# Performance work log

Measured on AMD Instinct MI355X. Metric: run time of the kernel, lower is better.

## Reference

```python
import jax, jax.numpy as jnp
import numpy as np

B, M, K, KNN = 2, 256, 64, 16
CXYZ, CFEAT = 3, 61
CIN = CXYZ + CFEAT  # 64
MLPS = [64, 128]
SUMM = sum(MLPS)    # 192
CALIB = 64
EXP = [256, 512]
OUT = 256
EPS = 1e-5


def bn(x, g, b):
    # BatchNorm eval mode with running_mean=0, running_var=1 (channel axis 1)
    shape = (1, -1) + (1,) * (x.ndim - 2)
    return x * (g / jnp.sqrt(1.0 + EPS)).reshape(shape) + b.reshape(shape)


def knn(x, k):
    xx = jnp.sum(x * x, axis=1)                      # (B, N)
    inner = jnp.einsum('bcn,bcm->bnm', x, x)         # (B, N, N)
    pd = 2.0 * inner - xx[:, :, None] - xx[:, None, :]
    return jax.lax.top_k(pd, k)[1]                   # (B, N, k)


def graph_feature(x, idx):
    # x: (B, C, N), idx: (B, N, k) -> (B, 2C, N, k)
    xt = jnp.transpose(x, (0, 2, 1))                 # (B, N, C)
    nb = jax.vmap(lambda a, i: a[i])(xt, idx)        # (B, N, k, C)
    ctr = xt[:, :, None, :]
    feat = jnp.concatenate([nb - ctr, jnp.broadcast_to(ctr, nb.shape)], axis=-1)
    return jnp.transpose(feat, (0, 3, 1, 2))


def forward(xyz, feats, e1_w, e1_g, e1_b, e2_w, e2_g, e2_b,
            cal1_w, cal1_g, cal1_b, cal2_w, cal2_bias,
            exp1_w, exp1_g, exp1_b, exp2_w, exp2_g, exp2_b,
            red_w, red_g, red_b, sc1_w, sc1_b, sc2_w, sc2_b,
            sc_n1_g, sc_n1_b, sc_n2_g, sc_n2_b):
    x3 = xyz.reshape(B * M, K, CXYZ).transpose(0, 2, 1)      # (BM, 3, K)
    f = feats.reshape(B * M, K, CFEAT).transpose(0, 2, 1)    # (BM, 61, K)
    idx = knn(x3, KNN)                                        # USE_FEATS_DIS=False: knn once on xyz
    x = jnp.concatenate([x3, f], axis=1)                      # (BM, 64, K)
    outs = []
    for W, g, b in ((e1_w, e1_g, e1_b), (e2_w, e2_g, e2_b)):
        gf = graph_feature(x, idx)                            # (BM, 2C, K, knn)
        y = jax.nn.relu(bn(jnp.einsum('oc,bcnk->bonk', W, gf), g, b))
        x = y.max(axis=-1)                                    # (BM, mlp_i, K)
        outs.append(x)
    x = jnp.concatenate(outs, axis=1)                         # (BM, 192, K)
    c = jax.nn.relu(bn(jnp.einsum('oc,bcn->bon', cal1_w, x), cal1_g, cal1_b))
    c = jnp.einsum('oc,bcn->bon', cal2_w, c) + cal2_bias[None, :, None]
    x = jax.nn.sigmoid(c) * x
    x = jax.nn.relu(bn(jnp.einsum('oc,bcn->bon', exp1_w, x), exp1_g, exp1_b))
    x = jax.nn.relu(bn(jnp.einsum('oc,bcn->bon', exp2_w, x), exp2_g, exp2_b))
    x = x.max(axis=-1).reshape(B, M, EXP[1]).transpose(0, 2, 1)  # (B, 512, M)
    x = jax.nn.relu(bn(jnp.einsum('oc,bcm->bom', red_w, x), red_g, red_b))
    x = bn(x + x, sc_n1_g, sc_n1_b)
    h = jax.nn.relu(jnp.einsum('oc,bcm->bom', sc1_w, x) + sc1_b[None, :, None])
    h = jnp.einsum('oc,bcm->bom', sc2_w, h) + sc2_b[None, :, None]
    x = bn(x + h, sc_n2_g, sc_n2_b)
    return x                                                  # (B, 256, M)


def setup_inputs() -> dict:
    key = jax.random.key(0)
    ks = jax.random.split(key, 16)
    w = lambda k, s: jax.random.normal(k, s, jnp.float32) * 0.05
    ones = lambda n: jnp.ones((n,), jnp.float32)
    zeros = lambda n: jnp.zeros((n,), jnp.float32)
    return {
        'xyz': jax.random.normal(ks[0], (B, M, K, CXYZ), jnp.float32),
        'feats': jax.random.normal(ks[1], (B, M, K, CFEAT), jnp.float32),
        'e1_w': w(ks[2], (MLPS[0], 2 * CIN)), 'e1_g': ones(MLPS[0]), 'e1_b': zeros(MLPS[0]),
        'e2_w': w(ks[3], (MLPS[1], 2 * MLPS[0])), 'e2_g': ones(MLPS[1]), 'e2_b': zeros(MLPS[1]),
        'cal1_w': w(ks[4], (CALIB, SUMM)), 'cal1_g': ones(CALIB), 'cal1_b': zeros(CALIB),
        'cal2_w': w(ks[5], (SUMM, CALIB)), 'cal2_bias': zeros(SUMM),
        'exp1_w': w(ks[6], (EXP[0], SUMM)), 'exp1_g': ones(EXP[0]), 'exp1_b': zeros(EXP[0]),
        'exp2_w': w(ks[7], (EXP[1], EXP[0])), 'exp2_g': ones(EXP[1]), 'exp2_b': zeros(EXP[1]),
        'red_w': w(ks[8], (OUT, EXP[1])), 'red_g': ones(OUT), 'red_b': zeros(OUT),
        'sc1_w': w(ks[9], (OUT, OUT)), 'sc1_b': zeros(OUT),
        'sc2_w': w(ks[10], (OUT, OUT)), 'sc2_b': zeros(OUT),
        'sc_n1_g': ones(OUT), 'sc_n1_b': zeros(OUT),
        'sc_n2_g': ones(OUT), 'sc_n2_b': zeros(OUT),
    }


def reference(xyz, feats, e1_w, e1_g, e1_b, e2_w, e2_g, e2_b,
              cal1_w, cal1_g, cal1_b, cal2_w, cal2_bias,
              exp1_w, exp1_g, exp1_b, exp2_w, exp2_g, exp2_b,
              red_w, red_g, red_b, sc1_w, sc1_b, sc2_w, sc2_b,
              sc_n1_g, sc_n1_b, sc_n2_g, sc_n2_b):
    return forward(xyz, feats, e1_w, e1_g, e1_b, e2_w, e2_g, e2_b,
                   cal1_w, cal1_g, cal1_b, cal2_w, cal2_bias,
                   exp1_w, exp1_g, exp1_b, exp2_w, exp2_g, exp2_b,
                   red_w, red_g, red_b, sc1_w, sc1_b, sc2_w, sc2_b,
                   sc_n1_g, sc_n1_b, sc_n2_g, sc_n2_b)
```

## Files before the change

kernel.cpp:

```cpp
#include <hip/hip_runtime.h>
#include <hip/hip_bf16.h>
#include <math.h>
#include <stddef.h>

#define DEV __device__ __forceinline__
__device__ const float BNS = 0.99999500003749968f;

typedef __bf16 bf16x8 __attribute__((ext_vector_type(8)));
typedef float  f32x4  __attribute__((ext_vector_type(4)));

#define MF(a,b,c) __builtin_amdgcn_mfma_f32_16x16x32_bf16(a,b,c,0,0,0)

DEV unsigned short f2bs(float v){
  union{ __hip_bfloat16 b; unsigned short u; } c; c.b=__float2bfloat16(v); return c.u;
}
DEV float bs2f(unsigned short u){
  union{ unsigned short u; __hip_bfloat16 b; } c; c.u=u; return __bfloat162float(c.b);
}

DEV void put_split(unsigned short* chunks, int n, int c, float v){
  unsigned short hv=f2bs(v), lv=f2bs(v-bs2f(hv));
  int cc=c>>5, u=(c>>3)&3, e=c&7;
  unsigned short* base = chunks + cc*4096;
  base[(n*8 + (u     ^ (n&7)))*8 + e] = hv;
  base[(n*8 + ((u+4) ^ (n&7)))*8 + e] = lv;
}
DEV float get_split(const unsigned short* chunks, int n, int c){
  int cc=c>>5, u=(c>>3)&3, e=c&7;
  const unsigned short* base = chunks + cc*4096;
  return bs2f(base[(n*8 + (u     ^ (n&7)))*8 + e])
       + bs2f(base[(n*8 + ((u+4) ^ (n&7)))*8 + e]);
}


__global__ __launch_bounds__(256) void k_prep(const float* __restrict__ e1_w,
    const float* __restrict__ e2_w, const float* __restrict__ cal1_w,
    const float* __restrict__ cal2_w, const float* __restrict__ exp1_w,
    const float* __restrict__ exp2_w, unsigned short* __restrict__ Whi,
    unsigned short* __restrict__ Wlo,
    const float* __restrict__ red_w, const float* __restrict__ sc1_w,
    const float* __restrict__ sc2_w, float* __restrict__ Wt_red,
    float* __restrict__ Wt_s1, float* __restrict__ Wt_s2){
  __shared__ float s[32][33];
  int bid = blockIdx.x;
  if(bid < 896){
    const float* src; unsigned short *hi,*lo; int mode, O=0, i0;
    if(bid<32)      { src=e1_w;  hi=Whi;       lo=Wlo;       mode=1; O= 64; i0=bid*256; }
    else if(bid<96) { src=e2_w;  hi=Whi+8192;  lo=Wlo+8192;  mode=1; O=128; i0=(bid-32)*256; }
    else if(bid<144){ src=cal1_w;hi=Whi+24576; lo=Wlo+24576; mode=0;        i0=(bid-96)*256; }
    else if(bid<192){ src=cal2_w;hi=Whi+36864; lo=Wlo+36864; mode=0;        i0=(bid-144)*256; }
    else if(bid<384){ src=exp1_w;hi=Whi+49152; lo=Wlo+49152; mode=0;        i0=(bid-192)*256; }
    else            { src=exp2_w;hi=Whi+98304; lo=Wlo+98304; mode=0;        i0=(bid-384)*256; }
    int i = i0 + threadIdx.x;
    float v;
    if(mode==0) v = src[i];
    else {
      int row=i>>6, c=i&63;
      v = (row<O) ? src[row*128+c] : (src[(row-O)*128+64+c]-src[(row-O)*128+c]);
    }
    unsigned short h=f2bs(v); hi[i]=h; lo[i]=f2bs(v-bs2f(h));
  } else {
    int lb = bid-896;
    const float* in; float* out; int O,K;
    if(lb<128){ in=red_w; out=Wt_red; O=256; K=512; }
    else if(lb<192){ in=sc1_w; out=Wt_s1; O=256; K=256; lb-=128; }
    else { in=sc2_w; out=Wt_s2; O=256; K=256; lb-=192; }
    int nt=O>>5;
    int to=lb%nt, tk=lb/nt;
    int c=threadIdx.x&31, r8=threadIdx.x>>5;
    #pragma unroll
    for(int p=0;p<4;p++){
      int r=r8+p*8;
      s[r][c]=in[(size_t)(to*32+r)*K + tk*32 + c];
    }
    __syncthreads();
    #pragma unroll
    for(int p=0;p<4;p++){
      int r=r8+p*8;
      out[(size_t)(tk*32+r)*O + to*32 + c]=s[c][r];
    }
  }
}

__global__ __launch_bounds__(256) void k_knne12(const float* __restrict__ xyz,
    const float* __restrict__ feats,
    const unsigned short* __restrict__ W1h, const unsigned short* __restrict__ W1l,
    const unsigned short* __restrict__ W2h, const unsigned short* __restrict__ W2l,
    const float* __restrict__ g1, const float* __restrict__ b1,
    const float* __restrict__ g2, const float* __restrict__ b2,
    unsigned short* __restrict__ cat){
  __shared__ float bufA[64*65];
  __shared__ float bufB[64*65];
  __shared__ __align__(16) unsigned short sb[64*136];
  __shared__ int   ips[64*16];
  __shared__ float sx0[64], sx1[64], sx2[64], sxx[64];
  int bm = blockIdx.x;
  int tid = threadIdx.x, n = tid&63, s = tid>>6;
  int wid = tid>>6, lane = tid&63;
  int l15 = lane&15, q = lane>>4;
  if(s==0){
    const float* xp = xyz + (size_t)(bm*64+n)*3;
    float px=xp[0], py=xp[1], pz=xp[2];
    sx0[n]=px; sx1[n]=py; sx2[n]=pz; sxx[n]=px*px+py*py+pz*pz;
  }
  __syncthreads();
  {
    int p = lane>>2, seg = lane&3;
    int n1 = wid*16 + p;
    float px=sx0[n1], py=sx1[n1], pz=sx2[n1], xxn=sxx[n1];
    float pdr[16];
    #pragma unroll
    for(int t=0;t<16;t++){
      int m = seg*16+t;
      pdr[t] = 2.f*(px*sx0[m]+py*sx1[m]+pz*sx2[m]) - xxn - sxx[m];
    }
    for(int j=0;j<16;j++){
      float bv=-3.4e38f; int bi=seg*16;
      #pragma unroll
      for(int t=0;t<16;t++){ if(pdr[t]>bv){bv=pdr[t]; bi=seg*16+t;} }
      float ov=__shfl_xor(bv,1); int oi=__shfl_xor(bi,1);
      if(ov>bv || (ov==bv && oi<bi)){bv=ov;bi=oi;}
      ov=__shfl_xor(bv,2); oi=__shfl_xor(bi,2);
      if(ov>bv || (ov==bv && oi<bi)){bv=ov;bi=oi;}
      if(seg==0) ips[n1*16+j]=bi;
      if((bi>>4)==seg) pdr[bi&15]=-3.4e38f;
    }
  }
  {
    unsigned short* r = sb + n*136;
    if(s==0){
      float px=sx0[n], py=sx1[n], pz=sx2[n];
      unsigned short h;
      h=f2bs(px); r[0]=h; r[64]=f2bs(px-bs2f(h));
      h=f2bs(py); r[1]=h; r[65]=f2bs(py-bs2f(h));
      h=f2bs(pz); r[2]=h; r[66]=f2bs(pz-bs2f(h));
    }
    const float* fp = feats + (size_t)(bm*64+n)*61;
    #pragma unroll
    for(int t=0;t<16;t++){
      int cc = s*16+t;
      if(cc<61){
        float v=fp[cc]; unsigned short h=f2bs(v);
        r[3+cc]=h; r[64+3+cc]=f2bs(v-bs2f(h));
      }
    }
  }
  __syncthreads();
  {
    int rbase = ((wid<2)?0:64) + (wid&1)*32;
    f32x4 acc[2][4];
    #pragma unroll
    for(int a=0;a<2;a++)
      #pragma unroll
      for(int d=0;d<4;d++) acc[a][d]=(f32x4){0.f,0.f,0.f,0.f};
    #pragma unroll
    for(int kc=0;kc<2;kc++){
      int k0=kc*32;
      size_t a0=(size_t)(rbase+l15)*64 + k0 + q*8;
      size_t a1=(size_t)(rbase+16+l15)*64 + k0 + q*8;
      bf16x8 a0h=*(const bf16x8*)(W1h+a0), a0l=*(const bf16x8*)(W1l+a0);
      bf16x8 a1h=*(const bf16x8*)(W1h+a1), a1l=*(const bf16x8*)(W1l+a1);
      #pragma unroll
      for(int nt=0;nt<4;nt++){
        int row = nt*16 + l15;
        bf16x8 bh = *(const bf16x8*)&sb[row*136 + k0 + q*8];
        bf16x8 bl = *(const bf16x8*)&sb[row*136 + 64 + k0 + q*8];
        acc[0][nt]=MF(a0h,bh,acc[0][nt]);
        acc[0][nt]=MF(a0h,bl,acc[0][nt]);
        acc[0][nt]=MF(a0l,bh,acc[0][nt]);
        acc[1][nt]=MF(a1h,bh,acc[1][nt]);
        acc[1][nt]=MF(a1h,bl,acc[1][nt]);
        acc[1][nt]=MF(a1l,bh,acc[1][nt]);
      }
    }
    __syncthreads();
    float* dst = (wid<2)? bufA : bufB;
    int ro = (wid&1)*32;
    #pragma unroll
    for(int mt=0;mt<2;mt++)
      #pragma unroll
      for(int nt=0;nt<4;nt++)
        #pragma unroll
        for(int rr=0;rr<4;rr++)
          dst[(ro+mt*16+q*4+rr)*65 + nt*16+l15] = acc[mt][nt][rr];
  }
  __syncthreads();
  {
    int o = lane;
    float sc = g1[o]*BNS, bi = b1[o];
    #pragma unroll 4
    for(int j=0;j<16;j++){
      int nn = wid*16 + j;
      const int* ip = &ips[nn*16];
      float mz = -3.4e38f;
      #pragma unroll
      for(int k=0;k<16;k++) mz = fmaxf(mz, bufA[o*65 + ip[k]]);
      float v = fmaxf(sc*(mz + bufB[o*65 + nn]) + bi, 0.f);
      unsigned short hv = f2bs(v), lv = f2bs(v - bs2f(hv));
      size_t cb = ((size_t)bm*64+nn)*384 + o;
      cat[cb] = hv; cat[cb+192] = lv;
      sb[nn*136 + o] = hv; sb[nn*136 + 64 + o] = lv;
    }
  }
  for(int ch=0; ch<2; ch++){
    __syncthreads();
    int rbase = ((wid<2)?0:128) + ch*64 + (wid&1)*32;
    f32x4 acc[2][4];
    #pragma unroll
    for(int a=0;a<2;a++)
      #pragma unroll
      for(int d=0;d<4;d++) acc[a][d]=(f32x4){0.f,0.f,0.f,0.f};
    #pragma unroll
    for(int kc=0;kc<2;kc++){
      int k0=kc*32;
      size_t a0=(size_t)(rbase+l15)*64 + k0 + q*8;
      size_t a1=(size_t)(rbase+16+l15)*64 + k0 + q*8;
      bf16x8 a0h=*(const bf16x8*)(W2h+a0), a0l=*(const bf16x8*)(W2l+a0);
      bf16x8 a1h=*(const bf16x8*)(W2h+a1), a1l=*(const bf16x8*)(W2l+a1);
      #pragma unroll
      for(int nt=0;nt<4;nt++){
        int row = nt*16 + l15;
        bf16x8 bh = *(const bf16x8*)&sb[row*136 + k0 + q*8];
        bf16x8 bl = *(const bf16x8*)&sb[row*136 + 64 + k0 + q*8];
        acc[0][nt]=MF(a0h,bh,acc[0][nt]);
        acc[0][nt]=MF(a0h,bl,acc[0][nt]);
        acc[0][nt]=MF(a0l,bh,acc[0][nt]);
        acc[1][nt]=MF(a1h,bh,acc[1][nt]);
        acc[1][nt]=MF(a1h,bl,acc[1][nt]);
        acc[1][nt]=MF(a1l,bh,acc[1][nt]);
      }
    }
    __syncthreads();
    float* dst = (wid<2)? bufA : bufB;
    int ro = (wid&1)*32;
    #pragma unroll
    for(int mt=0;mt<2;mt++)
      #pragma unroll
      for(int nt=0;nt<4;nt++)
        #pragma unroll
        for(int rr=0;rr<4;rr++)
          dst[(ro+mt*16+q*4+rr)*65 + nt*16+l15] = acc[mt][nt][rr];
    __syncthreads();
    int o = ch*64 + lane;
    float sc = g2[o]*BNS, bi = b2[o];
    #pragma unroll 4
    for(int j=0;j<16;j++){
      int nn = wid*16 + j;
      const int* ip = &ips[nn*16];
      float mz = -3.4e38f;
      #pragma unroll
      for(int k=0;k<16;k++) mz = fmaxf(mz, bufA[lane*65 + ip[k]]);
      float v = fmaxf(sc*(mz + bufB[lane*65 + nn]) + bi, 0.f);
      unsigned short hv = f2bs(v);
      size_t cb = ((size_t)bm*64+nn)*384 + 64 + o;
      cat[cb] = hv; cat[cb+192] = f2bs(v - bs2f(hv));
    }
  }
}

__global__ __launch_bounds__(512,4) void k_mlp(
    const unsigned short* __restrict__ Whi, const unsigned short* __restrict__ Wlo,
    const unsigned short* __restrict__ cats,
    const float* __restrict__ c1g, const float* __restrict__ c1b,
    const float* __restrict__ c2bias,
    const float* __restrict__ e1g, const float* __restrict__ e1b,
    const float* __restrict__ e2g, const float* __restrict__ e2b,
    float* __restrict__ pool){
  __shared__ __align__(16) unsigned short buf[8*4096];
  __shared__ __align__(16) unsigned short calB[2*4096];
  int bm = blockIdx.x;
  int tid = threadIdx.x, wid = tid>>6, lane = tid&63;
  int l15 = lane&15, q = lane>>4;
  size_t xb = (size_t)bm*24576;
  #pragma unroll
  for(int i=0;i<6;i++){
    int U = tid + i*512;
    int kc = U>>9, w = U&511, rr = w>>3, up = w&7, u = up ^ (rr&7);
    const unsigned short* src = cats + xb + (size_t)rr*384
      + (u<4 ? (kc*32 + u*8) : (192 + kc*32 + (u-4)*8));
    *(uint4*)&buf[kc*4096 + w*8] = *(const uint4*)src;
  }
  __syncthreads();
  {
    int ot = wid>>1, rh = wid&1;
    f32x4 a0={0.f,0.f,0.f,0.f}, a1={0.f,0.f,0.f,0.f};
    const unsigned short* wh = Whi + 24576;
    const unsigned short* wl = Wlo + 24576;
    #pragma unroll
    for(int kc=0;kc<6;kc++){
      size_t wo = (size_t)(ot*16+l15)*192 + kc*32 + q*8;
      bf16x8 ah=*(const bf16x8*)(wh+wo), al=*(const bf16x8*)(wl+wo);
      const unsigned short* cb = buf + kc*4096;
      int r0 = rh*32+l15, r1 = rh*32+16+l15;
      bf16x8 xh0=*(const bf16x8*)&cb[(r0*8+((  q)^(r0&7)))*8];
      bf16x8 xl0=*(const bf16x8*)&cb[(r0*8+((4+q)^(r0&7)))*8];
      bf16x8 xh1=*(const bf16x8*)&cb[(r1*8+((  q)^(r1&7)))*8];
      bf16x8 xl1=*(const bf16x8*)&cb[(r1*8+((4+q)^(r1&7)))*8];
      a0=MF(ah,xh0,a0); a1=MF(ah,xh1,a1);
      a0=MF(ah,xl0,a0); a1=MF(ah,xl1,a1);
      a0=MF(al,xh0,a0); a1=MF(al,xh1,a1);
    }
    float s[4], bb[4];
    #pragma unroll
    for(int rr=0;rr<4;rr++){ int c=ot*16+q*4+rr; s[rr]=c1g[c]*BNS; bb[rr]=c1b[c]; }
    #pragma unroll
    for(int rr=0;rr<4;rr++){
      int c=ot*16+q*4+rr;
      put_split(calB, rh*32+l15,    c, fmaxf(a0[rr]*s[rr]+bb[rr],0.f));
      put_split(calB, rh*32+16+l15, c, fmaxf(a1[rr]*s[rr]+bb[rr],0.f));
    }
  }
  __syncthreads();
  {
    f32x4 ac[6];
    #pragma unroll
    for(int i=0;i<6;i++) ac[i]=(f32x4){0.f,0.f,0.f,0.f};
    const unsigned short* wh = Whi + 36864;
    const unsigned short* wl = Wlo + 36864;
    #pragma unroll
    for(int kc=0;kc<2;kc++){
      const unsigned short* cb = calB + kc*4096;
      #pragma unroll
      for(int i=0;i<6;i++){
        int j = wid*6+i, ot=j>>2, nf=j&3;
        size_t wo=(size_t)(ot*16+l15)*64 + kc*32 + q*8;
        bf16x8 ah=*(const bf16x8*)(wh+wo), al=*(const bf16x8*)(wl+wo);
        int r=nf*16+l15;
        bf16x8 xh=*(const bf16x8*)&cb[(r*8+((  q)^(r&7)))*8];
        bf16x8 xl=*(const bf16x8*)&cb[(r*8+((4+q)^(r&7)))*8];
        ac[i]=MF(ah,xh,ac[i]); ac[i]=MF(ah,xl,ac[i]); ac[i]=MF(al,xh,ac[i]);
      }
    }
    #pragma unroll
    for(int i=0;i<6;i++){
      int j=wid*6+i, ot=j>>2, nf=j&3, n=nf*16+l15;
      #pragma unroll
      for(int rr=0;rr<4;rr++){
        int c=ot*16+q*4+rr;
        float gv = 1.f/(1.f+__expf(-(ac[i][rr]+c2bias[c])));
        put_split(buf, n, c, get_split(buf,n,c)*gv);
      }
    }
  }
  __syncthreads();
  {
    f32x4 ac[2][4];
    #pragma unroll
    for(int a=0;a<2;a++)
      #pragma unroll
      for(int d=0;d<4;d++) ac[a][d]=(f32x4){0.f,0.f,0.f,0.f};
    const unsigned short* wh=Whi+49152; const unsigned short* wl=Wlo+49152;
    int ob = wid*32;
    #pragma unroll 2
    for(int kc=0;kc<6;kc++){
      bf16x8 ah[2], al[2];
      #pragma unroll
      for(int mt=0;mt<2;mt++){
        size_t wo=(size_t)(ob+mt*16+l15)*192 + kc*32 + q*8;
        ah[mt]=*(const bf16x8*)(wh+wo); al[mt]=*(const bf16x8*)(wl+wo);
      }
      const unsigned short* cb = buf + kc*4096;
      #pragma unroll
      for(int nf=0;nf<4;nf++){
        int r=nf*16+l15;
        bf16x8 xh=*(const bf16x8*)&cb[(r*8+((  q)^(r&7)))*8];
        bf16x8 xl=*(const bf16x8*)&cb[(r*8+((4+q)^(r&7)))*8];
        ac[0][nf]=MF(ah[0],xh,ac[0][nf]); ac[1][nf]=MF(ah[1],xh,ac[1][nf]);
        ac[0][nf]=MF(ah[0],xl,ac[0][nf]); ac[1][nf]=MF(ah[1],xl,ac[1][nf]);
        ac[0][nf]=MF(al[0],xh,ac[0][nf]); ac[1][nf]=MF(al[1],xh,ac[1][nf]);
      }
    }
    __syncthreads();
    #pragma unroll
    for(int mt=0;mt<2;mt++){
      float s[4], bb[4];
      #pragma unroll
      for(int rr=0;rr<4;rr++){ int c=ob+mt*16+q*4+rr; s[rr]=e1g[c]*BNS; bb[rr]=e1b[c]; }
      #pragma unroll
      for(int nf=0;nf<4;nf++){
        int n=nf*16+l15;
        #pragma unroll
        for(int rr=0;rr<4;rr++){
          int c=ob+mt*16+q*4+rr;
          put_split(buf, n, c, fmaxf(ac[mt][nf][rr]*s[rr]+bb[rr],0.f));
        }
      }
    }
  }
  __syncthreads();
  {
    f32x4 ac[4][4];
    #pragma unroll
    for(int a=0;a<4;a++)
      #pragma unroll
      for(int d=0;d<4;d++) ac[a][d]=(f32x4){0.f,0.f,0.f,0.f};
    const unsigned short* wh=Whi+98304; const unsigned short* wl=Wlo+98304;
    int ob = wid*64;
    for(int kc=0;kc<8;kc++){
      bf16x8 ah[4], al[4];
      #pragma unroll
      for(int mt=0;mt<4;mt++){
        size_t wo=(size_t)(ob+mt*16+l15)*256 + kc*32 + q*8;
        ah[mt]=*(const bf16x8*)(wh+wo); al[mt]=*(const bf16x8*)(wl+wo);
      }
      const unsigned short* cb = buf + kc*4096;
      #pragma unroll
      for(int nf=0;nf<4;nf++){
        int r=nf*16+l15;
        bf16x8 xh=*(const bf16x8*)&cb[(r*8+((  q)^(r&7)))*8];
        bf16x8 xl=*(const bf16x8*)&cb[(r*8+((4+q)^(r&7)))*8];
        #pragma unroll
        for(int mt=0;mt<4;mt++) ac[mt][nf]=MF(ah[mt],xh,ac[mt][nf]);
        #pragma unroll
        for(int mt=0;mt<4;mt++) ac[mt][nf]=MF(ah[mt],xl,ac[mt][nf]);
        #pragma unroll
        for(int mt=0;mt<4;mt++) ac[mt][nf]=MF(al[mt],xh,ac[mt][nf]);
      }
    }
    int b = bm>>8, m = bm&255;
    #pragma unroll
    for(int mt=0;mt<4;mt++){
      float s[4], bb[4];
      #pragma unroll
      for(int rr=0;rr<4;rr++){ int c=ob+mt*16+q*4+rr; s[rr]=e2g[c]*BNS; bb[rr]=e2b[c]; }
      #pragma unroll
      for(int rr=0;rr<4;rr++){
        float v = ac[mt][0][rr]*s[rr]+bb[rr];
        v = fmaxf(v, ac[mt][1][rr]*s[rr]+bb[rr]);
        v = fmaxf(v, ac[mt][2][rr]*s[rr]+bb[rr]);
        v = fmaxf(v, ac[mt][3][rr]*s[rr]+bb[rr]);
        v = fmaxf(v, 0.f);
        v = fmaxf(v, __shfl_xor(v,1));
        v = fmaxf(v, __shfl_xor(v,2));
        v = fmaxf(v, __shfl_xor(v,4));
        v = fmaxf(v, __shfl_xor(v,8));
        if(l15==0) pool[((size_t)b*512 + ob+mt*16+q*4+rr)*256 + m] = v;
      }
    }
  }
}

__global__ __launch_bounds__(512) void k_headf(const float* __restrict__ Wt_red,
    const float* __restrict__ Wt_s1, const float* __restrict__ Wt_s2,
    const float* __restrict__ pool, float* __restrict__ Og,
    const float* __restrict__ red_g, const float* __restrict__ red_b,
    const float* __restrict__ n1g, const float* __restrict__ n1b,
    const float* __restrict__ s1b, const float* __restrict__ s2b,
    const float* __restrict__ n2g, const float* __restrict__ n2b){
  __shared__ float P[512*3];
  __shared__ float X1[256*3];
  __shared__ float H[256*3];
  __shared__ float PB[256*5];
  int g = blockIdx.x;
  int b = g>>7, mg = g&127;
  int m0 = mg*2;
  int tid = threadIdx.x;
  int o = tid&255, h = tid>>8;
  {
    int c = tid;
    float2 v = *(const float2*)&pool[((size_t)b*512+c)*256 + m0];
    P[c*3+0]=v.x; P[c*3+1]=v.y;
  }
  __syncthreads();
  float a0=0.f, a1=0.f;
  {
    int c0 = h*256;
    #pragma unroll 8
    for(int i=0;i<256;i++){
      int c = c0+i;
      float w = Wt_red[c*256+o];
      a0 += w*P[c*3]; a1 += w*P[c*3+1];
    }
  }
  PB[o*5+h*2]=a0; PB[o*5+h*2+1]=a1;
  __syncthreads();
  a0 = PB[o*5]+PB[o*5+2]; a1 = PB[o*5+1]+PB[o*5+3];
  float x0r,x1r;
  {
    float s=red_g[o]*BNS, bi=red_b[o], s1=n1g[o]*BNS, b1=n1b[o];
    float r0=fmaxf(a0*s+bi,0.f), r1=fmaxf(a1*s+bi,0.f);
    x0r=2.f*r0*s1+b1; x1r=2.f*r1*s1+b1;
    if(h==0){ X1[o*3]=x0r; X1[o*3+1]=x1r; }
  }
  __syncthreads();
  a0=0.f; a1=0.f;
  {
    int c0 = h*128;
    #pragma unroll 8
    for(int i=0;i<128;i++){
      int c = c0+i;
      float w = Wt_s1[c*256+o];
      a0 += w*X1[c*3]; a1 += w*X1[c*3+1];
    }
  }
  PB[o*5+h*2]=a0; PB[o*5+h*2+1]=a1;
  __syncthreads();
  a0 = PB[o*5]+PB[o*5+2]; a1 = PB[o*5+1]+PB[o*5+3];
  {
    float bi=s1b[o];
    if(h==0){ H[o*3]=fmaxf(a0+bi,0.f); H[o*3+1]=fmaxf(a1+bi,0.f); }
  }
  __syncthreads();
  a0=0.f; a1=0.f;
  {
    int c0 = h*128;
    #pragma unroll 8
    for(int i=0;i<128;i++){
      int c = c0+i;
      float w = Wt_s2[c*256+o];
      a0 += w*H[c*3]; a1 += w*H[c*3+1];
    }
  }
  PB[o*5+h*2]=a0; PB[o*5+h*2+1]=a1;
  __syncthreads();
  if(h==0){
    a0 = PB[o*5]+PB[o*5+2]; a1 = PB[o*5+1]+PB[o*5+3];
    float bi=s2b[o], s2=n2g[o]*BNS, b2=n2b[o];
    float v0=(x0r+a0+bi)*s2+b2, v1=(x1r+a1+bi)*s2+b2;
    *(float2*)&Og[((size_t)b*256+o)*256 + m0] = make_float2(v0,v1);
  }
}

extern "C" void kernel_launch(void* const* d_in, const int* in_sizes, int n_in,
                              void* d_out, int out_size, void* d_ws, size_t ws_size,
                              hipStream_t stream){
  const float* xyz     =(const float*)d_in[0];
  const float* feats   =(const float*)d_in[1];
  const float* e1_w    =(const float*)d_in[2];
  const float* e1_g    =(const float*)d_in[3];
  const float* e1_b    =(const float*)d_in[4];
  const float* e2_w    =(const float*)d_in[5];
  const float* e2_g    =(const float*)d_in[6];
  const float* e2_b    =(const float*)d_in[7];
  const float* cal1_w  =(const float*)d_in[8];
  const float* cal1_g  =(const float*)d_in[9];
  const float* cal1_b  =(const float*)d_in[10];
  const float* cal2_w  =(const float*)d_in[11];
  const float* cal2_bias=(const float*)d_in[12];
  const float* exp1_w  =(const float*)d_in[13];
  const float* exp1_g  =(const float*)d_in[14];
  const float* exp1_b  =(const float*)d_in[15];
  const float* exp2_w  =(const float*)d_in[16];
  const float* exp2_g  =(const float*)d_in[17];
  const float* exp2_b  =(const float*)d_in[18];
  const float* red_w   =(const float*)d_in[19];
  const float* red_g   =(const float*)d_in[20];
  const float* red_b   =(const float*)d_in[21];
  const float* sc1_w   =(const float*)d_in[22];
  const float* sc1_b   =(const float*)d_in[23];
  const float* sc2_w   =(const float*)d_in[24];
  const float* sc2_b   =(const float*)d_in[25];
  const float* sc_n1_g =(const float*)d_in[26];
  const float* sc_n1_b =(const float*)d_in[27];
  const float* sc_n2_g =(const float*)d_in[28];
  const float* sc_n2_b =(const float*)d_in[29];

  char* wsb=(char*)d_ws;
  unsigned short* cats=(unsigned short*)(wsb + 10485760);
  float*          pool=(float*)         (wsb + 69206016);
  unsigned short* Whi =(unsigned short*)(wsb + 75497472);
  unsigned short* Wlo =(unsigned short*)(wsb + 76021760);
  float*          Wt_red=(float*)       (wsb + 76546048);
  float*          Wt_s1 =(float*)       (wsb + 77070336);
  float*          Wt_s2 =(float*)       (wsb + 77332480);
  unsigned short* e1e_h=Whi;          unsigned short* e1e_l=Wlo;
  unsigned short* e2e_h=Whi+8192;     unsigned short* e2e_l=Wlo+8192;

  k_prep      <<<1152,256,0,stream>>>(e1_w,e2_w,cal1_w,cal2_w,exp1_w,exp2_w,Whi,Wlo,
                                      red_w,sc1_w,sc2_w,Wt_red,Wt_s1,Wt_s2);
  k_knne12    <<<512,256,0,stream>>>(xyz,feats,e1e_h,e1e_l,e2e_h,e2e_l,
                                     e1_g,e1_b,e2_g,e2_b,cats);
  k_mlp       <<<512,512,0,stream>>>(Whi,Wlo,cats,cal1_g,cal1_b,cal2_bias,
                                     exp1_g,exp1_b,exp2_g,exp2_b,pool);
  k_headf     <<<256,512,0,stream>>>(Wt_red,Wt_s1,Wt_s2,pool,(float*)d_out,
                                     red_g,red_b,sc_n1_g,sc_n1_b,sc1_b,sc2_b,sc_n2_g,sc_n2_b);
}
```

Measured before the change: 267.5 us.

## Prefetch weight fragments across k_mlp stages and vectorize split-bf16 LDS stores

Measured after the change: 264.7 us. No clear change (-1.1%).

```diff
diff --git a/kernel.cpp b/kernel.cpp
--- a/kernel.cpp
+++ b/kernel.cpp
@@ -18,18 +18,23 @@
   union{ unsigned short u; __hip_bfloat16 b; } c; c.u=u; return __bfloat162float(c.b);
 }
 
-DEV void put_split(unsigned short* chunks, int n, int c, float v){
-  unsigned short hv=f2bs(v), lv=f2bs(v-bs2f(hv));
-  int cc=c>>5, u=(c>>3)&3, e=c&7;
+DEV void put_split4(unsigned short* chunks, int n, int c0, const float* v){
+  int cc=c0>>5, u=(c0>>3)&3, e=c0&7;
   unsigned short* base = chunks + cc*4096;
-  base[(n*8 + (u     ^ (n&7)))*8 + e] = hv;
-  base[(n*8 + ((u+4) ^ (n&7)))*8 + e] = lv;
-}
-DEV float get_split(const unsigned short* chunks, int n, int c){
-  int cc=c>>5, u=(c>>3)&3, e=c&7;
+  unsigned short h0=f2bs(v[0]), h1=f2bs(v[1]), h2=f2bs(v[2]), h3=f2bs(v[3]);
+  ushort4 hq = make_ushort4(h0,h1,h2,h3);
+  ushort4 lq = make_ushort4(f2bs(v[0]-bs2f(h0)), f2bs(v[1]-bs2f(h1)),
+                            f2bs(v[2]-bs2f(h2)), f2bs(v[3]-bs2f(h3)));
+  *(ushort4*)&base[(n*8 + (u     ^ (n&7)))*8 + e] = hq;
+  *(ushort4*)&base[(n*8 + ((u+4) ^ (n&7)))*8 + e] = lq;
+}
+DEV void get_split4(const unsigned short* chunks, int n, int c0, float* v){
+  int cc=c0>>5, u=(c0>>3)&3, e=c0&7;
   const unsigned short* base = chunks + cc*4096;
-  return bs2f(base[(n*8 + (u     ^ (n&7)))*8 + e])
-       + bs2f(base[(n*8 + ((u+4) ^ (n&7)))*8 + e]);
+  ushort4 hq = *(const ushort4*)&base[(n*8 + (u     ^ (n&7)))*8 + e];
+  ushort4 lq = *(const ushort4*)&base[(n*8 + ((u+4) ^ (n&7)))*8 + e];
+  v[0]=bs2f(hq.x)+bs2f(lq.x); v[1]=bs2f(hq.y)+bs2f(lq.y);
+  v[2]=bs2f(hq.z)+bs2f(lq.z); v[3]=bs2f(hq.w)+bs2f(lq.w);
 }
 
 
@@ -271,6 +276,14 @@
   int bm = blockIdx.x;
   int tid = threadIdx.x, wid = tid>>6, lane = tid&63;
   int l15 = lane&15, q = lane>>4;
+
+  const unsigned short* w1h = Whi + 24576;
+  const unsigned short* w1l = Wlo + 24576;
+  int c1ot = wid>>1, c1rh = wid&1;
+  size_t c1wo0 = (size_t)(c1ot*16+l15)*192 + q*8;
+  bf16x8 cah = *(const bf16x8*)(w1h+c1wo0);
+  bf16x8 cal_ = *(const bf16x8*)(w1l+c1wo0);
+
   size_t xb = (size_t)bm*24576;
   #pragma unroll
   for(int i=0;i<6;i++){
@@ -281,83 +294,115 @@
     *(uint4*)&buf[kc*4096 + w*8] = *(const uint4*)src;
   }
   __syncthreads();
-  {
-    int ot = wid>>1, rh = wid&1;
-    f32x4 a0={0.f,0.f,0.f,0.f}, a1={0.f,0.f,0.f,0.f};
-    const unsigned short* wh = Whi + 24576;
-    const unsigned short* wl = Wlo + 24576;
+
+  f32x4 a0={0.f,0.f,0.f,0.f}, a1={0.f,0.f,0.f,0.f};
+  {
+    int r0 = c1rh*32+l15, r1 = c1rh*32+16+l15;
+    __builtin_amdgcn_s_setprio(1);
     #pragma unroll
     for(int kc=0;kc<6;kc++){
-      size_t wo = (size_t)(ot*16+l15)*192 + kc*32 + q*8;
-      bf16x8 ah=*(const bf16x8*)(wh+wo), al=*(const bf16x8*)(wl+wo);
+      bf16x8 nah, nal;
+      if(kc<5){
+        size_t wo = c1wo0 + (kc+1)*32;
+        nah=*(const bf16x8*)(w1h+wo); nal=*(const bf16x8*)(w1l+wo);
+      }
       const unsigned short* cb = buf + kc*4096;
-      int r0 = rh*32+l15, r1 = rh*32+16+l15;
       bf16x8 xh0=*(const bf16x8*)&cb[(r0*8+((  q)^(r0&7)))*8];
       bf16x8 xl0=*(const bf16x8*)&cb[(r0*8+((4+q)^(r0&7)))*8];
       bf16x8 xh1=*(const bf16x8*)&cb[(r1*8+((  q)^(r1&7)))*8];
       bf16x8 xl1=*(const bf16x8*)&cb[(r1*8+((4+q)^(r1&7)))*8];
-      a0=MF(ah,xh0,a0); a1=MF(ah,xh1,a1);
-      a0=MF(ah,xl0,a0); a1=MF(ah,xl1,a1);
-      a0=MF(al,xh0,a0); a1=MF(al,xh1,a1);
-    }
-    float s[4], bb[4];
-    #pragma unroll
-    for(int rr=0;rr<4;rr++){ int c=ot*16+q*4+rr; s[rr]=c1g[c]*BNS; bb[rr]=c1b[c]; }
-    #pragma unroll
-    for(int rr=0;rr<4;rr++){
-      int c=ot*16+q*4+rr;
-      put_split(calB, rh*32+l15,    c, fmaxf(a0[rr]*s[rr]+bb[rr],0.f));
-      put_split(calB, rh*32+16+l15, c, fmaxf(a1[rr]*s[rr]+bb[rr],0.f));
-    }
-  }
-  __syncthreads();
-  {
-    f32x4 ac[6];
-    #pragma unroll
-    for(int i=0;i<6;i++) ac[i]=(f32x4){0.f,0.f,0.f,0.f};
-    const unsigned short* wh = Whi + 36864;
-    const unsigned short* wl = Wlo + 36864;
-    #pragma unroll
-    for(int kc=0;kc<2;kc++){
-      const unsigned short* cb = calB + kc*4096;
+      a0=MF(cah,xh0,a0); a1=MF(cah,xh1,a1);
+      a0=MF(cah,xl0,a0); a1=MF(cah,xl1,a1);
+      a0=MF(cal_,xh0,a0); a1=MF(cal_,xh1,a1);
+      cah=nah; cal_=nal;
+    }
+    __builtin_amdgcn_s_setprio(0);
+  }
+  const unsigned short* w2h = Whi + 36864;
+  const unsigned short* w2l = Wlo + 36864;
+  bf16x8 c2h[6], c2l[6];
+  #pragma unroll
+  for(int i=0;i<6;i++){
+    int ot = (wid*6+i)>>2;
+    size_t wo=(size_t)(ot*16+l15)*64 + q*8;
+    c2h[i]=*(const bf16x8*)(w2h+wo); c2l[i]=*(const bf16x8*)(w2l+wo);
+  }
+  {
+    int c0 = c1ot*16+q*4;
+    float4 sg = *(const float4*)&c1g[c0];
+    float4 bb = *(const float4*)&c1b[c0];
+    float v0[4], v1[4];
+    v0[0]=fmaxf(a0[0]*sg.x*BNS+bb.x,0.f); v1[0]=fmaxf(a1[0]*sg.x*BNS+bb.x,0.f);
+    v0[1]=fmaxf(a0[1]*sg.y*BNS+bb.y,0.f); v1[1]=fmaxf(a1[1]*sg.y*BNS+bb.y,0.f);
+    v0[2]=fmaxf(a0[2]*sg.z*BNS+bb.z,0.f); v1[2]=fmaxf(a1[2]*sg.z*BNS+bb.z,0.f);
+    v0[3]=fmaxf(a0[3]*sg.w*BNS+bb.w,0.f); v1[3]=fmaxf(a1[3]*sg.w*BNS+bb.w,0.f);
+    put_split4(calB, c1rh*32+l15,    c0, v0);
+    put_split4(calB, c1rh*32+16+l15, c0, v1);
+  }
+  __syncthreads();
+  f32x4 ac[6];
+  #pragma unroll
+  for(int i=0;i<6;i++) ac[i]=(f32x4){0.f,0.f,0.f,0.f};
+  #pragma unroll
+  for(int kc=0;kc<2;kc++){
+    const unsigned short* cb = calB + kc*4096;
+    if(kc==1){
       #pragma unroll
       for(int i=0;i<6;i++){
-        int j = wid*6+i, ot=j>>2, nf=j&3;
-        size_t wo=(size_t)(ot*16+l15)*64 + kc*32 + q*8;
-        bf16x8 ah=*(const bf16x8*)(wh+wo), al=*(const bf16x8*)(wl+wo);
-        int r=nf*16+l15;
-        bf16x8 xh=*(const bf16x8*)&cb[(r*8+((  q)^(r&7)))*8];
-        bf16x8 xl=*(const bf16x8*)&cb[(r*8+((4+q)^(r&7)))*8];
-        ac[i]=MF(ah,xh,ac[i]); ac[i]=MF(ah,xl,ac[i]); ac[i]=MF(al,xh,ac[i]);
-      }
-    }
+        int ot = (wid*6+i)>>2;
+        size_t wo=(size_t)(ot*16+l15)*64 + 32 + q*8;
+        c2h[i]=*(const bf16x8*)(w2h+wo); c2l[i]=*(const bf16x8*)(w2l+wo);
+      }
+    }
+    __builtin_amdgcn_s_setprio(1);
     #pragma unroll
     for(int i=0;i<6;i++){
-      int j=wid*6+i, ot=j>>2, nf=j&3, n=nf*16+l15;
-      #pragma unroll
-      for(int rr=0;rr<4;rr++){
-        int c=ot*16+q*4+rr;
-        float gv = 1.f/(1.f+__expf(-(ac[i][rr]+c2bias[c])));
-        put_split(buf, n, c, get_split(buf,n,c)*gv);
-      }
-    }
-  }
-  __syncthreads();
-  {
-    f32x4 ac[2][4];
+      int nf=(wid*6+i)&3;
+      int r=nf*16+l15;
+      bf16x8 xh=*(const bf16x8*)&cb[(r*8+((  q)^(r&7)))*8];
+      bf16x8 xl=*(const bf16x8*)&cb[(r*8+((4+q)^(r&7)))*8];
+      ac[i]=MF(c2h[i],xh,ac[i]); ac[i]=MF(c2h[i],xl,ac[i]); ac[i]=MF(c2l[i],xh,ac[i]);
+    }
+    __builtin_amdgcn_s_setprio(0);
+  }
+  const unsigned short* e1wh=Whi+49152; const unsigned short* e1wl=Wlo+49152;
+  int ob1 = wid*32;
+  bf16x8 p1h[2], p1l[2];
+  #pragma unroll
+  for(int mt=0;mt<2;mt++){
+    size_t wo=(size_t)(ob1+mt*16+l15)*192 + q*8;
+    p1h[mt]=*(const bf16x8*)(e1wh+wo); p1l[mt]=*(const bf16x8*)(e1wl+wo);
+  }
+  #pragma unroll
+  for(int i=0;i<6;i++){
+    int j=wid*6+i, ot=j>>2, nf=j&3, n=nf*16+l15;
+    int c0=ot*16+q*4;
+    float4 cb4 = *(const float4*)&c2bias[c0];
+    float xv[4];
+    get_split4(buf, n, c0, xv);
+    xv[0] *= 1.f/(1.f+__expf(-(ac[i][0]+cb4.x)));
+    xv[1] *= 1.f/(1.f+__expf(-(ac[i][1]+cb4.y)));
+    xv[2] *= 1.f/(1.f+__expf(-(ac[i][2]+cb4.z)));
+    xv[3] *= 1.f/(1.f+__expf(-(ac[i][3]+cb4.w)));
+    put_split4(buf, n, c0, xv);
+  }
+  __syncthreads();
+  {
+    f32x4 e1a[2][4];
     #pragma unroll
     for(int a=0;a<2;a++)
       #pragma unroll
-      for(int d=0;d<4;d++) ac[a][d]=(f32x4){0.f,0.f,0.f,0.f};
-    const unsigned short* wh=Whi+49152; const unsigned short* wl=Wlo+49152;
-    int ob = wid*32;
-    #pragma unroll 2
+      for(int d=0;d<4;d++) e1a[a][d]=(f32x4){0.f,0.f,0.f,0.f};
+    __builtin_amdgcn_s_setprio(1);
+    #pragma unroll
     for(int kc=0;kc<6;kc++){
-      bf16x8 ah[2], al[2];
-      #pragma unroll
-      for(int mt=0;mt<2;mt++){
-        size_t wo=(size_t)(ob+mt*16+l15)*192 + kc*32 + q*8;
-        ah[mt]=*(const bf16x8*)(wh+wo); al[mt]=*(const bf16x8*)(wl+wo);
+      bf16x8 nh[2], nl[2];
+      if(kc<5){
+        #pragma unroll
+        for(int mt=0;mt<2;mt++){
+          size_t wo=(size_t)(ob1+mt*16+l15)*192 + (kc+1)*32 + q*8;
+          nh[mt]=*(const bf16x8*)(e1wh+wo); nl[mt]=*(const bf16x8*)(e1wl+wo);
+        }
       }
       const unsigned short* cb = buf + kc*4096;
       #pragma unroll
@@ -365,76 +410,103 @@
         int r=nf*16+l15;
         bf16x8 xh=*(const bf16x8*)&cb[(r*8+((  q)^(r&7)))*8];
         bf16x8 xl=*(const bf16x8*)&cb[(r*8+((4+q)^(r&7)))*8];
-        ac[0][nf]=MF(ah[0],xh,ac[0][nf]); ac[1][nf]=MF(ah[1],xh,ac[1][nf]);
-        ac[0][nf]=MF(ah[0],xl,ac[0][nf]); ac[1][nf]=MF(ah[1],xl,ac[1][nf]);
-        ac[0][nf]=MF(al[0],xh,ac[0][nf]); ac[1][nf]=MF(al[1],xh,ac[1][nf]);
-      }
-    }
+        e1a[0][nf]=MF(p1h[0],xh,e1a[0][nf]); e1a[1][nf]=MF(p1h[1],xh,e1a[1][nf]);
+        e1a[0][nf]=MF(p1h[0],xl,e1a[0][nf]); e1a[1][nf]=MF(p1h[1],xl,e1a[1][nf]);
+        e1a[0][nf]=MF(p1l[0],xh,e1a[0][nf]); e1a[1][nf]=MF(p1l[1],xh,e1a[1][nf]);
+      }
+      p1h[0]=nh[0]; p1h[1]=nh[1]; p1l[0]=nl[0]; p1l[1]=nl[1];
+    }
+    __builtin_amdgcn_s_setprio(0);
     __syncthreads();
+    const unsigned short* e2wh=Whi+98304; const unsigned short* e2wl=Wlo+98304;
+    int ob2 = wid*64;
+    bf16x8 p2h[4], p2l[4];
+    #pragma unroll
+    for(int mt=0;mt<4;mt++){
+      size_t wo=(size_t)(ob2+mt*16+l15)*256 + q*8;
+      p2h[mt]=*(const bf16x8*)(e2wh+wo); p2l[mt]=*(const bf16x8*)(e2wl+wo);
+    }
     #pragma unroll
     for(int mt=0;mt<2;mt++){
-      float s[4], bb[4];
-      #pragma unroll
-      for(int rr=0;rr<4;rr++){ int c=ob+mt*16+q*4+rr; s[rr]=e1g[c]*BNS; bb[rr]=e1b[c]; }
+      int c0 = ob1+mt*16+q*4;
+      float4 sg = *(const float4*)&e1g[c0];
+      float4 bb = *(const float4*)&e1b[c0];
       #pragma unroll
       for(int nf=0;nf<4;nf++){
-        int n=nf*16+l15;
-        #pragma unroll
-        for(int rr=0;rr<4;rr++){
-          int c=ob+mt*16+q*4+rr;
-          put_split(buf, n, c, fmaxf(ac[mt][nf][rr]*s[rr]+bb[rr],0.f));
-        }
-      }
-    }
-  }
-  __syncthreads();
-  {
-    f32x4 ac[4][4];
+        float v[4];
+        v[0]=fmaxf(e1a[mt][nf][0]*sg.x*BNS+bb.x,0.f);
+        v[1]=fmaxf(e1a[mt][nf][1]*sg.y*BNS+bb.y,0.f);
+        v[2]=fmaxf(e1a[mt][nf][2]*sg.z*BNS+bb.z,0.f);
+        v[3]=fmaxf(e1a[mt][nf][3]*sg.w*BNS+bb.w,0.f);
+        put_split4(buf, nf*16+l15, c0, v);
+      }
+    }
+    __syncthreads();
+    f32x4 a2[4][4];
     #pragma unroll
     for(int a=0;a<4;a++)
       #pragma unroll
-      for(int d=0;d<4;d++) ac[a][d]=(f32x4){0.f,0.f,0.f,0.f};
-    const unsigned short* wh=Whi+98304; const unsigned short* wl=Wlo+98304;
-    int ob = wid*64;
-    for(int kc=0;kc<8;kc++){
-      bf16x8 ah[4], al[4];
-      #pragma unroll
-      for(int mt=0;mt<4;mt++){
-        size_t wo=(size_t)(ob+mt*16+l15)*256 + kc*32 + q*8;
-        ah[mt]=*(const bf16x8*)(wh+wo); al[mt]=*(const bf16x8*)(wl+wo);
-      }
-      const unsigned short* cb = buf + kc*4096;
+      for(int d=0;d<4;d++) a2[a][d]=(f32x4){0.f,0.f,0.f,0.f};
+    {
+      const unsigned short* cb = buf;
+      __builtin_amdgcn_s_setprio(1);
       #pragma unroll
       for(int nf=0;nf<4;nf++){
         int r=nf*16+l15;
         bf16x8 xh=*(const bf16x8*)&cb[(r*8+((  q)^(r&7)))*8];
         bf16x8 xl=*(const bf16x8*)&cb[(r*8+((4+q)^(r&7)))*8];
         #pragma unroll
-        for(int mt=0;mt<4;mt++) ac[mt][nf]=MF(ah[mt],xh,ac[mt][nf]);
-        #pragma unroll
-        for(int mt=0;mt<4;mt++) ac[mt][nf]=MF(ah[mt],xl,ac[mt][nf]);
-        #pragma unroll
-        for(int mt=0;mt<4;mt++) ac[mt][nf]=MF(al[mt],xh,ac[mt][nf]);
-      }
+        for(int mt=0;mt<4;mt++) a2[mt][nf]=MF(p2h[mt],xh,a2[mt][nf]);
+        #pragma unroll
+        for(int mt=0;mt<4;mt++) a2[mt][nf]=MF(p2h[mt],xl,a2[mt][nf]);
+        #pragma unroll
+        for(int mt=0;mt<4;mt++) a2[mt][nf]=MF(p2l[mt],xh,a2[mt][nf]);
+      }
+      __builtin_amdgcn_s_setprio(0);
+    }
+    for(int kc=1;kc<8;kc++){
+      bf16x8 ch[4], cl[4];
+      #pragma unroll
+      for(int mt=0;mt<4;mt++){
+        size_t wo=(size_t)(ob2+mt*16+l15)*256 + kc*32 + q*8;
+        ch[mt]=*(const bf16x8*)(e2wh+wo); cl[mt]=*(const bf16x8*)(e2wl+wo);
+      }
+      const unsigned short* cb = buf + kc*4096;
+      __builtin_amdgcn_s_setprio(1);
+      #pragma unroll
+      for(int nf=0;nf<4;nf++){
+        int r=nf*16+l15;
+        bf16x8 xh=*(const bf16x8*)&cb[(r*8+((  q)^(r&7)))*8];
+        bf16x8 xl=*(const bf16x8*)&cb[(r*8+((4+q)^(r&7)))*8];
+        #pragma unroll
+        for(int mt=0;mt<4;mt++) a2[mt][nf]=MF(ch[mt],xh,a2[mt][nf]);
+        #pragma unroll
+        for(int mt=0;mt<4;mt++) a2[mt][nf]=MF(ch[mt],xl,a2[mt][nf]);
+        #pragma unroll
+        for(int mt=0;mt<4;mt++) a2[mt][nf]=MF(cl[mt],xh,a2[mt][nf]);
+      }
+      __builtin_amdgcn_s_setprio(0);
     }
     int b = bm>>8, m = bm&255;
     #pragma unroll
     for(int mt=0;mt<4;mt++){
-      float s[4], bb[4];
-      #pragma unroll
-      for(int rr=0;rr<4;rr++){ int c=ob+mt*16+q*4+rr; s[rr]=e2g[c]*BNS; bb[rr]=e2b[c]; }
+      int c0 = ob2+mt*16+q*4;
+      float4 sg = *(const float4*)&e2g[c0];
+      float4 bb = *(const float4*)&e2b[c0];
+      float s[4]={sg.x*BNS,sg.y*BNS,sg.z*BNS,sg.w*BNS};
+      float bbv[4]={bb.x,bb.y,bb.z,bb.w};
       #pragma unroll
       for(int rr=0;rr<4;rr++){
-        float v = ac[mt][0][rr]*s[rr]+bb[rr];
-        v = fmaxf(v, ac[mt][1][rr]*s[rr]+bb[rr]);
-        v = fmaxf(v, ac[mt][2][rr]*s[rr]+bb[rr]);
-        v = fmaxf(v, ac[mt][3][rr]*s[rr]+bb[rr]);
+        float v = a2[mt][0][rr]*s[rr]+bbv[rr];
+        v = fmaxf(v, a2[mt][1][rr]*s[rr]+bbv[rr]);
+        v = fmaxf(v, a2[mt][2][rr]*s[rr]+bbv[rr]);
+        v = fmaxf(v, a2[mt][3][rr]*s[rr]+bbv[rr]);
         v = fmaxf(v, 0.f);
         v = fmaxf(v, __shfl_xor(v,1));
         v = fmaxf(v, __shfl_xor(v,2));
         v = fmaxf(v, __shfl_xor(v,4));
         v = fmaxf(v, __shfl_xor(v,8));
-        if(l15==0) pool[((size_t)b*512 + ob+mt*16+q*4+rr)*256 + m] = v;
+        if(l15==0) pool[((size_t)b*512 + c0+rr)*256 + m] = v;
       }
     }
   }
```
